# Kernel tuning notes

Measured on AMD Instinct MI355X. Metric: run time of the kernel, lower is better.

The kernel has to match this reference:

```python
import jax, jax.numpy as jnp
import numpy as np

NUM_TOKENS = 2048  # = token_limit(0.5) * seq_len(4096)


def setup_inputs() -> dict:
    key = jax.random.key(0)
    k0, k1, k2, k3 = jax.random.split(key, 4)
    B, S, D, F = 4, 4096, 2048, 8192
    return {
        "x": jax.random.normal(k0, (B, S, D), dtype=jnp.float32),
        "Wp": jax.random.normal(k1, (D, 1), dtype=jnp.float32) * (1.0 / np.sqrt(D)),
        "bp": jnp.zeros((1,), dtype=jnp.float32),
        "W1": jax.random.normal(k2, (D, F), dtype=jnp.float32) * (1.0 / np.sqrt(D)),
        "b1": jnp.zeros((F,), dtype=jnp.float32),
        "W2": jax.random.normal(k3, (F, D), dtype=jnp.float32) * (1.0 / np.sqrt(F)),
        "b2": jnp.zeros((D,), dtype=jnp.float32),
    }


def reference(x, Wp, bp, W1, b1, W2, b2):
    # Router: per-token scalar score via Linear(dim, 1)
    weights = x @ Wp + bp                      # [B, S, 1]
    # Faithful to source: softmax over dim=-1 (size-1 axis -> all ones)
    weights = jax.nn.softmax(weights, axis=-1)  # [B, S, 1]
    scores = weights[..., 0]                   # [B, S]
    # top-k token selection along the sequence axis
    _, idx = jax.lax.top_k(scores, NUM_TOKENS)  # [B, k] int32
    # gather the selected full tokens (intended semantics of the expand+gather)
    topk_tokens = jnp.take_along_axis(x, idx[:, :, None], axis=1)  # [B, k, D]
    # downstream block: transformer FFN
    h = jax.nn.gelu(topk_tokens @ W1 + b1)     # [B, k, 4D]
    out = h @ W2 + b2                          # [B, k, D]
    return out
```

## Files before the change

kernel.cpp:

```cpp
#include <hip/hip_runtime.h>
#include <hip/hip_bf16.h>

typedef unsigned int u32;
typedef unsigned short u16;

using bf16x8 = __attribute__((ext_vector_type(8))) short;
using f32x4  = __attribute__((ext_vector_type(4))) float;

#define DEVI static __device__ __forceinline__

DEVI u16 f2bf(float f) {
  __hip_bfloat16 h = __float2bfloat16(f);
  union { __hip_bfloat16 h; u16 u; } v; v.h = h;
  return v.u;
}

__global__ void k_convert_x(const float* __restrict__ x, u16* __restrict__ xb) {
  int idx = blockIdx.x * blockDim.x + threadIdx.x;
  size_t e = (size_t)idx * 4;
  int row = (int)(e >> 11);
  int d   = (int)(e & 2047);
  int b = row >> 11, t = row & 2047;
  const float4 v = *reinterpret_cast<const float4*>(
      x + ((size_t)(b * 4096 + t) * 2048 + d));
  ushort4 o;
  o.x = f2bf(v.x); o.y = f2bf(v.y); o.z = f2bf(v.z); o.w = f2bf(v.w);
  *reinterpret_cast<ushort4*>(xb + (size_t)row * 2048 + d) = o;
}

__global__ void k_transpose_bf16(const float* __restrict__ in,
                                 u16* __restrict__ out, int R, int C) {
  __shared__ u16 lds[64][66];
  const int t = threadIdx.x;
  const int tile_r = blockIdx.y * 64;
  const int tile_c = blockIdx.x * 64;
  const int cc = (t & 15) * 4;
  const int r0 = t >> 4;
#pragma unroll
  for (int i = 0; i < 4; ++i) {
    int r = r0 + i * 16;
    const float4 v = *reinterpret_cast<const float4*>(
        in + (size_t)(tile_r + r) * C + tile_c + cc);
    lds[r][cc]     = f2bf(v.x);
    lds[r][cc + 1] = f2bf(v.y);
    lds[r][cc + 2] = f2bf(v.z);
    lds[r][cc + 3] = f2bf(v.w);
  }
  __syncthreads();
  const int rr = (t & 15) * 4;
  const int c0 = t >> 4;
#pragma unroll
  for (int i = 0; i < 4; ++i) {
    int c = c0 + i * 16;
    ushort4 o;
    o.x = lds[rr][c]; o.y = lds[rr + 1][c];
    o.z = lds[rr + 2][c]; o.w = lds[rr + 3][c];
    *reinterpret_cast<ushort4*>(out + (size_t)(tile_c + c) * R + tile_r + rr) = o;
  }
}

#define GLDS16(g, l)                                                          \
  __builtin_amdgcn_global_load_lds(                                           \
      (const __attribute__((address_space(1))) u32*)(g),                      \
      (__attribute__((address_space(3))) u32*)(l), 16, 0, 0)

template <int DO_GELU, int BNPART>
DEVI void gemm_body(u16* lds, const u16* __restrict__ A,
                    const u16* __restrict__ B, const float* __restrict__ bias,
                    void* __restrict__ Cout, int N, int K, int nbn, int sft) {
  const int bid = blockIdx.x;
  int bm, bn;
  if (BNPART) {
    const int local = bid >> 3;
    bn = ((bid & 7) << sft) + (local & ((1 << sft) - 1));
    bm = local >> sft;
  } else {
    const int wg = (bid & 7) * (gridDim.x >> 3) + (bid >> 3);
    bm = wg / nbn; bn = wg % nbn;
  }

  const int tid  = threadIdx.x;
  const int w    = tid >> 6, lane = tid & 63;
  const int wr   = w >> 2, wcol = w & 3;
  const int l15  = lane & 15, lhi = lane >> 4;

  const size_t arow0 = (size_t)bm * 256;
  const size_t brow0 = (size_t)bn * 256;

  const int srow  = tid >> 3;
  const int scolb = ((tid & 7) * 16) ^ ((srow & 7) << 4);
  const u16* pA = A + (arow0 + srow) * (size_t)K + (scolb >> 1);
  const u16* pB = B + (brow0 + srow) * (size_t)K + (scolb >> 1);
  const int wA = w * 512;

  const u32 arow_b = (u32)((wr * 128 + l15) * 128);
  const u32 brow_b = (u32)((wcol * 64 + l15) * 128);
  const u32 axor   = (u32)((lhi * 16) ^ ((l15 & 7) << 4));
  const char* ldsb = (const char*)lds;

  f32x4 acc[8][4] = {};
  const int nk = K >> 6;

#define STAGE_PAIR(KT, PB, C)                                                 \
  do {                                                                        \
    GLDS16(pA + (size_t)(KT) * 64 + (size_t)(C) * 64 * (size_t)K,             \
           lds + (PB) * 16384 + (C) * 4096 + wA);                             \
    GLDS16(pB + (size_t)(KT) * 64 + (size_t)(C) * 64 * (size_t)K,             \
           lds + 32768 + (PB) * 16384 + (C) * 4096 + wA);                     \
  } while (0)

#define READ_A(DST, MH, ABASE)                                                \
  _Pragma("unroll") for (int m2 = 0; m2 < 4; ++m2)                            \
  _Pragma("unroll") for (int kk = 0; kk < 2; ++kk)                            \
    DST[m2][kk] = *(const bf16x8*)(ldsb + (ABASE) + arow_b +                  \
                                   ((MH)*4 + m2) * 2048 + (axor ^ (kk << 6)));

#define READ_B(DST, NH, BBASE)                                                \
  _Pragma("unroll") for (int n2 = 0; n2 < 2; ++n2)                            \
  _Pragma("unroll") for (int kk = 0; kk < 2; ++kk)                            \
    DST[n2][kk] = *(const bf16x8*)(ldsb + (BBASE) + brow_b +                  \
                                   ((NH)*2 + n2) * 2048 + (axor ^ (kk << 6)));

#define MFMA_Q(MH, NH, AREG, BREG)                                            \
  _Pragma("unroll") for (int m2 = 0; m2 < 4; ++m2)                            \
  _Pragma("unroll") for (int n2 = 0; n2 < 2; ++n2)                            \
  _Pragma("unroll") for (int kk = 0; kk < 2; ++kk)                            \
    acc[(MH)*4 + m2][(NH)*2 + n2] = __builtin_amdgcn_mfma_f32_16x16x32_bf16(  \
        AREG[m2][kk], BREG[n2][kk], acc[(MH)*4 + m2][(NH)*2 + n2], 0, 0, 0);

  STAGE_PAIR(0, 0, 0); STAGE_PAIR(0, 0, 1);
  STAGE_PAIR(0, 0, 2); STAGE_PAIR(0, 0, 3);
  if (nk > 1) {
    STAGE_PAIR(1, 1, 0); STAGE_PAIR(1, 1, 1);
    asm volatile("s_waitcnt vmcnt(4)" ::: "memory");
  } else {
    asm volatile("s_waitcnt vmcnt(0)" ::: "memory");
  }
  __builtin_amdgcn_s_barrier();

  for (int kt = 0; kt < nk; ++kt) {
    const int p = kt & 1;
    const u32 abase = (u32)p * 32768u;
    const u32 bbase = 65536u + (u32)p * 32768u;
    bf16x8 a0[4][2], a1[4][2], b0[2][2], b1[2][2];

    READ_A(a0, 0, abase);
    READ_B(b0, 0, bbase);
    READ_B(b1, 1, bbase);
    READ_A(a1, 1, abase);
    __builtin_amdgcn_sched_barrier(0);

    __builtin_amdgcn_s_setprio(1);
    MFMA_Q(0, 0, a0, b0);
    MFMA_Q(0, 1, a0, b1);
    __builtin_amdgcn_s_setprio(0);

    asm volatile("s_waitcnt lgkmcnt(0)" ::: "memory");
    __builtin_amdgcn_s_barrier();
    __builtin_amdgcn_sched_barrier(0);

    if (kt + 1 < nk) { STAGE_PAIR(kt + 1, p ^ 1, 2); STAGE_PAIR(kt + 1, p ^ 1, 3); }
    if (kt + 2 < nk) { STAGE_PAIR(kt + 2, p, 0); STAGE_PAIR(kt + 2, p, 1); }

    __builtin_amdgcn_s_setprio(1);
    MFMA_Q(1, 1, a1, b1);
    MFMA_Q(1, 0, a1, b0);
    __builtin_amdgcn_s_setprio(0);

    if (kt + 2 < nk) {
      asm volatile("s_waitcnt vmcnt(4)" ::: "memory");
    } else {
      asm volatile("s_waitcnt vmcnt(0)" ::: "memory");
    }
    __builtin_amdgcn_s_barrier();
  }

  const int colb = (int)brow0 + wcol * 64;
  float bb[4];
#pragma unroll
  for (int n = 0; n < 4; ++n) bb[n] = bias[colb + n * 16 + l15];
  const int tr = lane >> 2, tc = (lane & 3) * 16;

  if (DO_GELU) {
    u16* slot = lds + (size_t)w * 1152;
#pragma unroll
    for (int m = 0; m < 8; ++m) {
      const int rowb = (int)arow0 + wr * 128 + m * 16;
#pragma unroll
      for (int n = 0; n < 4; ++n)
#pragma unroll
        for (int r = 0; r < 4; ++r) {
          float v = acc[m][n][r] + bb[n];
          float u2 = v * (1.5957691216f + 0.0713548162f * v * v);
          float g  = v / (1.f + __expf(-u2));
          slot[(lhi * 4 + r) * 72 + n * 16 + l15] = f2bf(g);
        }
      asm volatile("s_waitcnt lgkmcnt(0)" ::: "memory");
      uint4 d0 = *(const uint4*)(slot + tr * 72 + tc);
      uint4 d1 = *(const uint4*)(slot + tr * 72 + tc + 8);
      u16* gp = (u16*)Cout + (size_t)(rowb + tr) * N + colb + tc;
      *(uint4*)gp = d0;
      *(uint4*)(gp + 8) = d1;
      asm volatile("s_waitcnt lgkmcnt(0)" ::: "memory");
    }
  } else {
    float* slotf = (float*)(void*)lds + (size_t)w * 1088;
#pragma unroll
    for (int m = 0; m < 8; ++m) {
      const int rowb = (int)arow0 + wr * 128 + m * 16;
#pragma unroll
      for (int n = 0; n < 4; ++n)
#pragma unroll
        for (int r = 0; r < 4; ++r)
          slotf[(lhi * 4 + r) * 68 + n * 16 + l15] = acc[m][n][r] + bb[n];
      asm volatile("s_waitcnt lgkmcnt(0)" ::: "memory");
      float4 f0 = *(const float4*)(slotf + tr * 68 + tc);
      float4 f1 = *(const float4*)(slotf + tr * 68 + tc + 4);
      float4 f2 = *(const float4*)(slotf + tr * 68 + tc + 8);
      float4 f3 = *(const float4*)(slotf + tr * 68 + tc + 12);
      float* gp = (float*)Cout + (size_t)(rowb + tr) * N + colb + tc;
      *(float4*)gp = f0;
      *(float4*)(gp + 4) = f1;
      *(float4*)(gp + 8) = f2;
      *(float4*)(gp + 12) = f3;
      asm volatile("s_waitcnt lgkmcnt(0)" ::: "memory");
    }
  }
#undef STAGE_PAIR
#undef READ_A
#undef READ_B
#undef MFMA_Q
}

__global__ __launch_bounds__(512, 2) void k_ffn1(
    const u16* __restrict__ A, const u16* __restrict__ B,
    const float* __restrict__ bias, void* __restrict__ Cout,
    int N, int K, int nbn, int sft) {
  __shared__ __align__(64) u16 lds[65536];
  gemm_body<1, 1>(lds, A, B, bias, Cout, N, K, nbn, sft);
}

__global__ __launch_bounds__(512, 2) void k_ffn2(
    const u16* __restrict__ A, const u16* __restrict__ B,
    const float* __restrict__ bias, void* __restrict__ Cout,
    int N, int K, int nbn, int sft) {
  __shared__ __align__(64) u16 lds[65536];
  gemm_body<0, 0>(lds, A, B, bias, Cout, N, K, nbn, sft);
}

extern "C" void kernel_launch(void* const* d_in, const int* in_sizes, int n_in,
                              void* d_out, int out_size, void* d_ws,
                              size_t ws_size, hipStream_t stream) {
  const float* x  = (const float*)d_in[0];
  const float* W1 = (const float*)d_in[3];
  const float* b1 = (const float*)d_in[4];
  const float* W2 = (const float*)d_in[5];
  const float* b2 = (const float*)d_in[6];
  float* out = (float*)d_out;

  char* ws = (char*)d_ws;
  u16* Xb  = (u16*)(ws);
  u16* W1T = (u16*)(ws + 33554432);
  u16* W2T = (u16*)(ws + 67108864);
  u16* H   = (u16*)(ws + 100663296);

  k_convert_x<<<16384, 256, 0, stream>>>(x, Xb);
  k_transpose_bf16<<<dim3(8192 / 64, 2048 / 64), 256, 0, stream>>>(W1, W1T, 2048, 8192);
  k_transpose_bf16<<<dim3(2048 / 64, 8192 / 64), 256, 0, stream>>>(W2, W2T, 8192, 2048);
  k_ffn1<<<1024, 512, 0, stream>>>(Xb, W1T, b1, (void*)H, 8192, 2048, 32, 2);
  k_ffn2<<<256, 512, 0, stream>>>(H, W2T, b2, (void*)out, 2048, 8192, 8, 0);
}
```

Baseline: 579.8 us.

## Reschedule FFN GEMM pipelines with finer MFMA phases and earlier prefetch

Result: faster. 549.0 us (-5.3%).

```diff
diff --git a/kernel.cpp b/kernel.cpp
--- a/kernel.cpp
+++ b/kernel.cpp
@@ -64,43 +64,6 @@
       (const __attribute__((address_space(1))) u32*)(g),                      \
       (__attribute__((address_space(3))) u32*)(l), 16, 0, 0)
 
-template <int DO_GELU, int BNPART>
-DEVI void gemm_body(u16* lds, const u16* __restrict__ A,
-                    const u16* __restrict__ B, const float* __restrict__ bias,
-                    void* __restrict__ Cout, int N, int K, int nbn, int sft) {
-  const int bid = blockIdx.x;
-  int bm, bn;
-  if (BNPART) {
-    const int local = bid >> 3;
-    bn = ((bid & 7) << sft) + (local & ((1 << sft) - 1));
-    bm = local >> sft;
-  } else {
-    const int wg = (bid & 7) * (gridDim.x >> 3) + (bid >> 3);
-    bm = wg / nbn; bn = wg % nbn;
-  }
-
-  const int tid  = threadIdx.x;
-  const int w    = tid >> 6, lane = tid & 63;
-  const int wr   = w >> 2, wcol = w & 3;
-  const int l15  = lane & 15, lhi = lane >> 4;
-
-  const size_t arow0 = (size_t)bm * 256;
-  const size_t brow0 = (size_t)bn * 256;
-
-  const int srow  = tid >> 3;
-  const int scolb = ((tid & 7) * 16) ^ ((srow & 7) << 4);
-  const u16* pA = A + (arow0 + srow) * (size_t)K + (scolb >> 1);
-  const u16* pB = B + (brow0 + srow) * (size_t)K + (scolb >> 1);
-  const int wA = w * 512;
-
-  const u32 arow_b = (u32)((wr * 128 + l15) * 128);
-  const u32 brow_b = (u32)((wcol * 64 + l15) * 128);
-  const u32 axor   = (u32)((lhi * 16) ^ ((l15 & 7) << 4));
-  const char* ldsb = (const char*)lds;
-
-  f32x4 acc[8][4] = {};
-  const int nk = K >> 6;
-
 #define STAGE_PAIR(KT, PB, C)                                                 \
   do {                                                                        \
     GLDS16(pA + (size_t)(KT) * 64 + (size_t)(C) * 64 * (size_t)K,             \
@@ -128,14 +91,50 @@
     acc[(MH)*4 + m2][(NH)*2 + n2] = __builtin_amdgcn_mfma_f32_16x16x32_bf16(  \
         AREG[m2][kk], BREG[n2][kk], acc[(MH)*4 + m2][(NH)*2 + n2], 0, 0, 0);
 
+#define LGKM0_SBAR()                                                          \
+  do {                                                                        \
+    asm volatile("s_waitcnt lgkmcnt(0)" ::: "memory");                        \
+    __builtin_amdgcn_sched_barrier(0);                                        \
+  } while (0)
+
+__global__ __launch_bounds__(512, 2) void k_ffn1(
+    const u16* __restrict__ A, const u16* __restrict__ B,
+    const float* __restrict__ bias, u16* __restrict__ Cout,
+    int N, int K, int sft) {
+  __shared__ __align__(64) u16 lds[65536];
+
+  const int bid   = blockIdx.x;
+  const int local = bid >> 3;
+  const int bn    = ((bid & 7) << sft) + (local & ((1 << sft) - 1));
+  const int bm    = local >> sft;
+
+  const int tid  = threadIdx.x;
+  const int w    = tid >> 6, lane = tid & 63;
+  const int wr   = w >> 2, wcol = w & 3;
+  const int l15  = lane & 15, lhi = lane >> 4;
+
+  const size_t arow0 = (size_t)bm * 256;
+  const size_t brow0 = (size_t)bn * 256;
+
+  const int srow  = tid >> 3;
+  const int scolb = ((tid & 7) * 16) ^ ((srow & 7) << 4);
+  const u16* pA = A + (arow0 + srow) * (size_t)K + (scolb >> 1);
+  const u16* pB = B + (brow0 + srow) * (size_t)K + (scolb >> 1);
+  const int wA = w * 512;
+
+  const u32 arow_b = (u32)((wr * 128 + l15) * 128);
+  const u32 brow_b = (u32)((wcol * 64 + l15) * 128);
+  const u32 axor   = (u32)((lhi * 16) ^ ((l15 & 7) << 4));
+  const char* ldsb = (const char*)lds;
+
+  f32x4 acc[8][4] = {};
+  const int nk = K >> 6;
+
   STAGE_PAIR(0, 0, 0); STAGE_PAIR(0, 0, 1);
   STAGE_PAIR(0, 0, 2); STAGE_PAIR(0, 0, 3);
-  if (nk > 1) {
-    STAGE_PAIR(1, 1, 0); STAGE_PAIR(1, 1, 1);
-    asm volatile("s_waitcnt vmcnt(4)" ::: "memory");
-  } else {
-    asm volatile("s_waitcnt vmcnt(0)" ::: "memory");
-  }
+  STAGE_PAIR(1, 1, 0); STAGE_PAIR(1, 1, 1);
+  STAGE_PAIR(1, 1, 2); STAGE_PAIR(1, 1, 3);
+  asm volatile("s_waitcnt vmcnt(8)" ::: "memory");
   __builtin_amdgcn_s_barrier();
 
   for (int kt = 0; kt < nk; ++kt) {
@@ -143,11 +142,123 @@
     const u32 abase = (u32)p * 32768u;
     const u32 bbase = 65536u + (u32)p * 32768u;
     bf16x8 a0[4][2], a1[4][2], b0[2][2], b1[2][2];
+    const bool st2 = (kt + 2 < nk);
+
+    READ_A(a0, 0, abase);
+    READ_B(b0, 0, bbase);
+    __builtin_amdgcn_s_barrier();
+    LGKM0_SBAR();
+    __builtin_amdgcn_s_setprio(1);
+    MFMA_Q(0, 0, a0, b0);
+    __builtin_amdgcn_s_setprio(0);
+    __builtin_amdgcn_s_barrier();
+
+    READ_B(b1, 1, bbase);
+    __builtin_amdgcn_s_barrier();
+    LGKM0_SBAR();
+    __builtin_amdgcn_s_setprio(1);
+    MFMA_Q(0, 1, a0, b1);
+    __builtin_amdgcn_s_setprio(0);
+    __builtin_amdgcn_s_barrier();
+
+    READ_A(a1, 1, abase);
+    if (st2) { STAGE_PAIR(kt + 2, p, 0); STAGE_PAIR(kt + 2, p, 2); }
+    __builtin_amdgcn_s_barrier();
+    LGKM0_SBAR();
+    __builtin_amdgcn_s_setprio(1);
+    MFMA_Q(1, 1, a1, b1);
+    __builtin_amdgcn_s_setprio(0);
+    __builtin_amdgcn_s_barrier();
+
+    if (st2) { STAGE_PAIR(kt + 2, p, 1); STAGE_PAIR(kt + 2, p, 3); }
+    __builtin_amdgcn_sched_barrier(0);
+    __builtin_amdgcn_s_setprio(1);
+    MFMA_Q(1, 0, a1, b0);
+    __builtin_amdgcn_s_setprio(0);
+    if (st2) {
+      asm volatile("s_waitcnt vmcnt(8)" ::: "memory");
+    } else {
+      asm volatile("s_waitcnt vmcnt(0)" ::: "memory");
+    }
+    __builtin_amdgcn_s_barrier();
+  }
+
+  const int colb = (int)brow0 + wcol * 64;
+  float bb[4];
+#pragma unroll
+  for (int n = 0; n < 4; ++n) bb[n] = bias[colb + n * 16 + l15];
+  const int tr = lane >> 2, tc = (lane & 3) * 16;
+  u16* slot = lds + (size_t)w * 1152;
+#pragma unroll
+  for (int m = 0; m < 8; ++m) {
+    const int rowb = (int)arow0 + wr * 128 + m * 16;
+#pragma unroll
+    for (int n = 0; n < 4; ++n)
+#pragma unroll
+      for (int r = 0; r < 4; ++r) {
+        float v = acc[m][n][r] + bb[n];
+        float u2 = v * (1.5957691216f + 0.0713548162f * v * v);
+        float g  = v / (1.f + __expf(-u2));
+        slot[(lhi * 4 + r) * 72 + n * 16 + l15] = f2bf(g);
+      }
+    asm volatile("s_waitcnt lgkmcnt(0)" ::: "memory");
+    uint4 d0 = *(const uint4*)(slot + tr * 72 + tc);
+    uint4 d1 = *(const uint4*)(slot + tr * 72 + tc + 8);
+    u16* gp = Cout + (size_t)(rowb + tr) * N + colb + tc;
+    *(uint4*)gp = d0;
+    *(uint4*)(gp + 8) = d1;
+    asm volatile("s_waitcnt lgkmcnt(0)" ::: "memory");
+  }
+}
+
+__global__ __launch_bounds__(512, 2) void k_ffn2(
+    const u16* __restrict__ A, const u16* __restrict__ B,
+    const float* __restrict__ bias, float* __restrict__ Cout,
+    int N, int K, int nbn) {
+  __shared__ __align__(64) u16 lds[65536];
+
+  const int bid = blockIdx.x;
+  const int wg  = (bid & 7) * (gridDim.x >> 3) + (bid >> 3);
+  const int bm = wg / nbn, bn = wg % nbn;
+
+  const int tid  = threadIdx.x;
+  const int w    = tid >> 6, lane = tid & 63;
+  const int wr   = w >> 2, wcol = w & 3;
+  const int l15  = lane & 15, lhi = lane >> 4;
+
+  const size_t arow0 = (size_t)bm * 256;
+  const size_t brow0 = (size_t)bn * 256;
+  const int srow  = tid >> 3;
+  const int scolb = ((tid & 7) * 16) ^ ((srow & 7) << 4);
+  const u16* pA = A + (arow0 + srow) * (size_t)K + (scolb >> 1);
+  const u16* pB = B + (brow0 + srow) * (size_t)K + (scolb >> 1);
+  const int wA = w * 512;
+
+  const u32 arow_b = (u32)((wr * 128 + l15) * 128);
+  const u32 brow_b = (u32)((wcol * 64 + l15) * 128);
+  const u32 axor   = (u32)((lhi * 16) ^ ((l15 & 7) << 4));
+  const char* ldsb = (const char*)lds;
+  const int nk = K >> 6;
+
+  STAGE_PAIR(0, 0, 0); STAGE_PAIR(0, 0, 1);
+  STAGE_PAIR(0, 0, 2); STAGE_PAIR(0, 0, 3);
+  STAGE_PAIR(1, 1, 0); STAGE_PAIR(1, 1, 1);
+  asm volatile("s_waitcnt vmcnt(4)" ::: "memory");
+  __builtin_amdgcn_s_barrier();
+
+  f32x4 acc[8][4] = {};
+
+  for (int kt = 0; kt < nk; ++kt) {
+    const int p = kt & 1;
+    const u32 abase = (u32)p * 32768u;
+    const u32 bbase = 65536u + (u32)p * 32768u;
+    bf16x8 a0[4][2], a1[4][2], b0[2][2], b1[2][2];
 
     READ_A(a0, 0, abase);
     READ_B(b0, 0, bbase);
     READ_B(b1, 1, bbase);
     READ_A(a1, 1, abase);
+    if (kt + 1 < nk) { STAGE_PAIR(kt + 1, p ^ 1, 2); STAGE_PAIR(kt + 1, p ^ 1, 3); }
     __builtin_amdgcn_sched_barrier(0);
 
     __builtin_amdgcn_s_setprio(1);
@@ -158,8 +269,6 @@
     asm volatile("s_waitcnt lgkmcnt(0)" ::: "memory");
     __builtin_amdgcn_s_barrier();
     __builtin_amdgcn_sched_barrier(0);
-
-    if (kt + 1 < nk) { STAGE_PAIR(kt + 1, p ^ 1, 2); STAGE_PAIR(kt + 1, p ^ 1, 3); }
     if (kt + 2 < nk) { STAGE_PAIR(kt + 2, p, 0); STAGE_PAIR(kt + 2, p, 1); }
 
     __builtin_amdgcn_s_setprio(1);
@@ -180,72 +289,27 @@
 #pragma unroll
   for (int n = 0; n < 4; ++n) bb[n] = bias[colb + n * 16 + l15];
   const int tr = lane >> 2, tc = (lane & 3) * 16;
-
-  if (DO_GELU) {
-    u16* slot = lds + (size_t)w * 1152;
-#pragma unroll
-    for (int m = 0; m < 8; ++m) {
-      const int rowb = (int)arow0 + wr * 128 + m * 16;
-#pragma unroll
-      for (int n = 0; n < 4; ++n)
-#pragma unroll
-        for (int r = 0; r < 4; ++r) {
-          float v = acc[m][n][r] + bb[n];
-          float u2 = v * (1.5957691216f + 0.0713548162f * v * v);
-          float g  = v / (1.f + __expf(-u2));
-          slot[(lhi * 4 + r) * 72 + n * 16 + l15] = f2bf(g);
-        }
-      asm volatile("s_waitcnt lgkmcnt(0)" ::: "memory");
-      uint4 d0 = *(const uint4*)(slot + tr * 72 + tc);
-      uint4 d1 = *(const uint4*)(slot + tr * 72 + tc + 8);
-      u16* gp = (u16*)Cout + (size_t)(rowb + tr) * N + colb + tc;
-      *(uint4*)gp = d0;
-      *(uint4*)(gp + 8) = d1;
-      asm volatile("s_waitcnt lgkmcnt(0)" ::: "memory");
-    }
-  } else {
-    float* slotf = (float*)(void*)lds + (size_t)w * 1088;
-#pragma unroll
-    for (int m = 0; m < 8; ++m) {
-      const int rowb = (int)arow0 + wr * 128 + m * 16;
-#pragma unroll
-      for (int n = 0; n < 4; ++n)
-#pragma unroll
-        for (int r = 0; r < 4; ++r)
-          slotf[(lhi * 4 + r) * 68 + n * 16 + l15] = acc[m][n][r] + bb[n];
-      asm volatile("s_waitcnt lgkmcnt(0)" ::: "memory");
-      float4 f0 = *(const float4*)(slotf + tr * 68 + tc);
-      float4 f1 = *(const float4*)(slotf + tr * 68 + tc + 4);
-      float4 f2 = *(const float4*)(slotf + tr * 68 + tc + 8);
-      float4 f3 = *(const float4*)(slotf + tr * 68 + tc + 12);
-      float* gp = (float*)Cout + (size_t)(rowb + tr) * N + colb + tc;
-      *(float4*)gp = f0;
-      *(float4*)(gp + 4) = f1;
-      *(float4*)(gp + 8) = f2;
-      *(float4*)(gp + 12) = f3;
-      asm volatile("s_waitcnt lgkmcnt(0)" ::: "memory");
-    }
-  }
-#undef STAGE_PAIR
-#undef READ_A
-#undef READ_B
-#undef MFMA_Q
-}
-
-__global__ __launch_bounds__(512, 2) void k_ffn1(
-    const u16* __restrict__ A, const u16* __restrict__ B,
-    const float* __restrict__ bias, void* __restrict__ Cout,
-    int N, int K, int nbn, int sft) {
-  __shared__ __align__(64) u16 lds[65536];
-  gemm_body<1, 1>(lds, A, B, bias, Cout, N, K, nbn, sft);
-}
-
-__global__ __launch_bounds__(512, 2) void k_ffn2(
-    const u16* __restrict__ A, const u16* __restrict__ B,
-    const float* __restrict__ bias, void* __restrict__ Cout,
-    int N, int K, int nbn, int sft) {
-  __shared__ __align__(64) u16 lds[65536];
-  gemm_body<0, 0>(lds, A, B, bias, Cout, N, K, nbn, sft);
+  float* slotf = (float*)(void*)lds + (size_t)w * 1088;
+#pragma unroll
+  for (int m = 0; m < 8; ++m) {
+    const int rowb = (int)arow0 + wr * 128 + m * 16;
+#pragma unroll
+    for (int n = 0; n < 4; ++n)
+#pragma unroll
+      for (int r = 0; r < 4; ++r)
+        slotf[(lhi * 4 + r) * 68 + n * 16 + l15] = acc[m][n][r] + bb[n];
+    asm volatile("s_waitcnt lgkmcnt(0)" ::: "memory");
+    float4 f0 = *(const float4*)(slotf + tr * 68 + tc);
+    float4 f1 = *(const float4*)(slotf + tr * 68 + tc + 4);
+    float4 f2 = *(const float4*)(slotf + tr * 68 + tc + 8);
+    float4 f3 = *(const float4*)(slotf + tr * 68 + tc + 12);
+    float* gp = Cout + (size_t)(rowb + tr) * N + colb + tc;
+    *(float4*)gp = f0;
+    *(float4*)(gp + 4) = f1;
+    *(float4*)(gp + 8) = f2;
+    *(float4*)(gp + 12) = f3;
+    asm volatile("s_waitcnt lgkmcnt(0)" ::: "memory");
+  }
 }
 
 extern "C" void kernel_launch(void* const* d_in, const int* in_sizes, int n_in,
@@ -267,6 +331,6 @@
   k_convert_x<<<16384, 256, 0, stream>>>(x, Xb);
   k_transpose_bf16<<<dim3(8192 / 64, 2048 / 64), 256, 0, stream>>>(W1, W1T, 2048, 8192);
   k_transpose_bf16<<<dim3(2048 / 64, 8192 / 64), 256, 0, stream>>>(W2, W2T, 8192, 2048);
-  k_ffn1<<<1024, 512, 0, stream>>>(Xb, W1T, b1, (void*)H, 8192, 2048, 32, 2);
-  k_ffn2<<<256, 512, 0, stream>>>(H, W2T, b2, (void*)out, 2048, 8192, 8, 0);
-}
+  k_ffn1<<<1024, 512, 0, stream>>>(Xb, W1T, b1, H, 8192, 2048, 2);
+  k_ffn2<<<256, 512, 0, stream>>>(H, W2T, b2, out, 2048, 8192, 8);
+}
```
